# Kernel tuning notes

Measured on AMD Instinct MI355X. Metric: run time of the kernel, lower is better.

Reference implementation:

```python
import jax, jax.numpy as jnp
import numpy as np

N = 1024
FD = 40   # feat dim = out_dim1 + out_dim1//4
EPS = 1e-7


def _lin(key, din, dout):
    return jax.random.normal(key, (din, dout), jnp.float32) * (1.0 / np.sqrt(din))


def setup_inputs() -> dict:
    key = jax.random.key(0)
    ks = jax.random.split(key, 16)
    pc = jax.random.normal(ks[0], (1, N, 3), jnp.float32)
    nrm = jax.random.normal(ks[1], (1, N, 3), jnp.float32)
    pc_normal = nrm / (jnp.linalg.norm(nrm, axis=-1, keepdims=True) + EPS)
    feat = jax.random.normal(ks[2], (1, N, FD), jnp.float32) * 0.1
    # pairwise distance matrix, as precomputed upstream in the repo
    dist = jnp.linalg.norm(pc[:, :, None, :] - pc[:, None, :, :], axis=-1)
    z = lambda d: jnp.zeros((d,), jnp.float32)
    return {
        'pc': pc, 'pc_normal': pc_normal, 'dist': dist, 'feat': feat,
        'l0_fc0_w': _lin(ks[3], 84, 32), 'l0_fc0_b': z(32),
        'l0_fc1_w': _lin(ks[4], 84, 32), 'l0_fc1_b': z(32),
        'l0_fc2_w': _lin(ks[5], 32, 32), 'l0_fc2_b': z(32),
        'l1_fc1_w': _lin(ks[6], 32, 32), 'l1_fc1_b': z(32),
        'l1_fc2_w': _lin(ks[7], 32, 32), 'l1_fc2_b': z(32),
        'l2_fc0_w': _lin(ks[8], 32, 16), 'l2_fc0_b': z(16),
        'l2_fc1_w': _lin(ks[9], 32, 16), 'l2_fc1_b': z(16),
        'l2_fc2_w': _lin(ks[10], 16, 16), 'l2_fc2_b': z(16),
        'final_w': _lin(ks[11], 16, 66), 'final_b': z(66),
    }


def _res_layer(x, fc1w, fc1b, fc2w, fc2b, fc0w=None, fc0b=None):
    x_res = x if fc0w is None else x @ fc0w + fc0b
    h = jax.nn.relu(x @ fc1w + fc1b)
    return h @ fc2w + fc2b + x_res


def reference(pc, pc_normal, dist, feat,
              l0_fc0_w, l0_fc0_b, l0_fc1_w, l0_fc1_b, l0_fc2_w, l0_fc2_b,
              l1_fc1_w, l1_fc1_b, l1_fc2_w, l1_fc2_b,
              l2_fc0_w, l2_fc0_b, l2_fc1_w, l2_fc1_b, l2_fc2_w, l2_fc2_b,
              final_w, final_b):
    B, n, _ = pc.shape
    # pairwise displacement, normalized by precomputed dist (torch chunking is
    # pure memory management; the math over the full [B,N,N] block is identical)
    xx = pc[:, :, None, :] - pc[:, None, :, :]            # [B,N,N,3]
    xx_normed = xx / (dist[..., None] + EPS)
    n_i = pc_normal[:, :, None, :]                        # query normals
    n_j = pc_normal[:, None, :, :]                        # key normals
    ppf = jnp.concatenate([
        jnp.sum(n_i * xx_normed, -1, keepdims=True),
        jnp.sum(n_j * xx_normed, -1, keepdims=True),
        jnp.sum(n_i * n_j, -1, keepdims=True),
        dist[..., None],
    ], -1)                                                # [B,N,N,4]
    f_i = jnp.broadcast_to(feat[:, :, None, :], (B, n, n, FD))
    f_j = jnp.broadcast_to(feat[:, None, :, :], (B, n, n, FD))
    x = jnp.concatenate([f_i, f_j, ppf], -1)              # [B,N,N,84]
    x = _res_layer(x, l0_fc1_w, l0_fc1_b, l0_fc2_w, l0_fc2_b, l0_fc0_w, l0_fc0_b)
    x = _res_layer(x, l1_fc1_w, l1_fc1_b, l1_fc2_w, l1_fc2_b)
    x = _res_layer(x, l2_fc1_w, l2_fc1_b, l2_fc2_w, l2_fc2_b, l2_fc0_w, l2_fc0_b)
    return x @ final_w + final_b                          # [B,N,N,66]
```

## Files before the change

kernel.cpp:

```cpp
#include <hip/hip_runtime.h>
#include <hip/hip_bf16.h>

#define NPTS 1024
#define EPSF 1e-7f

typedef const float* fp;
typedef __attribute__((ext_vector_type(8))) short short8;
typedef __attribute__((ext_vector_type(4))) float float4v;

#define OFF_B0   32768
#define OFF_A1   65536
#define OFF_B1   98304
#define OFF_FRAG 131072
#define OFF_W0PT 134656
#define OFF_W1PT 134784

static __device__ __forceinline__ short f2bf(float x) {
    __hip_bfloat16 h = __float2bfloat16(x);
    short s; __builtin_memcpy(&s, &h, 2); return s;
}
static __device__ __forceinline__ void lds_fence() {
    __asm__ volatile("s_waitcnt lgkmcnt(0)" ::: "memory");
}

__global__ __launch_bounds__(128) void ppf_pre(
    fp feat, fp w0, fp b0, fp w1, fp b1,
    fp l0w2, fp l1w1, fp l1w2, fp l2w0, fp l2w1, fp l2w2, fp fw,
    float* __restrict__ ws)
{
    const int bid = blockIdx.x;
    const int t = threadIdx.x;
    if (bid < 1024) {
        __shared__ float f[40];
        int p = bid;
        if (t < 40) f[t] = feat[p * 40 + t];
        __syncthreads();
        int g = t >> 5;
        int c = t & 31;
        fp W = (g < 2) ? w0 : w1;
        int rowoff = (g & 1) ? 40 : 0;
        float acc = 0.f;
        if (!(g & 1)) acc = (g < 2) ? b0[c] : b1[c];
        #pragma unroll
        for (int k = 0; k < 40; ++k)
            acc += f[k] * W[(rowoff + k) * 32 + c];
        ws[g * 32768 + p * 32 + c] = acc;
    } else if (bid < 1038) {
        int ff = bid - 1024;
        if (t >= 64) return;
        const float* src; int Kr, Nw, n0;
        switch (ff) {
            case 0:  src = l0w2; Kr = 32; Nw = 32; n0 = 0;  break;
            case 1:  src = l0w2; Kr = 32; Nw = 32; n0 = 16; break;
            case 2:  src = l1w1; Kr = 32; Nw = 32; n0 = 0;  break;
            case 3:  src = l1w1; Kr = 32; Nw = 32; n0 = 16; break;
            case 4:  src = l1w2; Kr = 32; Nw = 32; n0 = 0;  break;
            case 5:  src = l1w2; Kr = 32; Nw = 32; n0 = 16; break;
            case 6:  src = l2w0; Kr = 32; Nw = 16; n0 = 0;  break;
            case 7:  src = l2w1; Kr = 32; Nw = 16; n0 = 0;  break;
            case 8:  src = l2w2; Kr = 16; Nw = 16; n0 = 0;  break;
            default: src = fw;   Kr = 16; Nw = 66; n0 = (ff - 9) * 16; break;
        }
        int q = t >> 4;
        int n = n0 + (t & 15);
        unsigned dw[4];
        #pragma unroll
        for (int w = 0; w < 4; ++w) {
            unsigned short e[2];
            #pragma unroll
            for (int v = 0; v < 2; ++v) {
                int k = q * 8 + w * 2 + v;
                float val = (k < Kr && n < Nw) ? src[k * Nw + n] : 0.f;
                short s = f2bf(val);
                __builtin_memcpy(&e[v], &s, 2);
            }
            dw[w] = (unsigned)e[0] | ((unsigned)e[1] << 16);
        }
        unsigned* dst = (unsigned*)ws + OFF_FRAG + ff * 256 + t * 4;
        #pragma unroll
        for (int w = 0; w < 4; ++w) dst[w] = dw[w];
    } else if (bid == 1038) {
        ws[OFF_W0PT + t] = w0[(80 + (t & 3)) * 32 + (t >> 2)];
    } else {
        ws[OFF_W1PT + t] = w1[(80 + (t & 3)) * 32 + (t >> 2)];
    }
}

static __device__ __forceinline__ float4v mfma16(short8 a, short8 b, float4v c) {
    return __builtin_amdgcn_mfma_f32_16x16x32_bf16(a, b, c, 0, 0, 0);
}

__global__ __launch_bounds__(256) void ppf_main(
    fp pc, fp nrm, fp dist,
    fp l0b2, fp l1b1, fp l1b2, fp l2b0, fp l2b1, fp l2b2, fp fb,
    const float* __restrict__ ws, float* __restrict__ out)
{
    __shared__ __align__(16) float lds[4 * 1152];
    const int tid  = threadIdx.x;
    const int wv   = tid >> 6;
    const int lane = tid & 63;
    const int q    = lane >> 4;
    const int ml   = lane & 15;
    const int kb   = q * 8;
    float* xt = &lds[wv * 1152];
    float* ht = xt + 576;

    const int i    = blockIdx.x >> 2;
    const int jblk = ((blockIdx.x & 3) << 8) + (wv << 6);

    const short8* fragp = (const short8*)(ws + OFF_FRAG);
    const short8 fg_l0w2_0 = fragp[0 * 64 + lane], fg_l0w2_1 = fragp[1 * 64 + lane];
    const short8 fg_l1w1_0 = fragp[2 * 64 + lane], fg_l1w1_1 = fragp[3 * 64 + lane];
    const short8 fg_l1w2_0 = fragp[4 * 64 + lane], fg_l1w2_1 = fragp[5 * 64 + lane];
    const short8 fg_l2w0   = fragp[6 * 64 + lane];
    const short8 fg_l2w1   = fragp[7 * 64 + lane];
    const short8 fg_l2w2   = fragp[8 * 64 + lane];
    const short8 fg_fw0 = fragp[9 * 64 + lane],  fg_fw1 = fragp[10 * 64 + lane];
    const short8 fg_fw2 = fragp[11 * 64 + lane], fg_fw3 = fragp[12 * 64 + lane];
    const short8 fg_fw4 = fragp[13 * 64 + lane];

    const float4v* a0p = (const float4v*)(ws + i * 32 + kb);
    const float4v a0lo = a0p[0], a0hi = a0p[1];
    const float4v* a1p = (const float4v*)(ws + OFF_A1 + i * 32 + kb);
    const float4v a1lo = a1p[0], a1hi = a1p[1];
    const float4v* b2p = (const float4v*)(l0b2 + kb);
    const float4v b2lo = b2p[0], b2hi = b2p[1];
    float4v w0t[8], w1t[8];
    {
        const float4v* w0ptp = (const float4v*)(ws + OFF_W0PT + kb * 4);
        const float4v* w1ptp = (const float4v*)(ws + OFF_W1PT + kb * 4);
        #pragma unroll
        for (int jj = 0; jj < 8; ++jj) { w0t[jj] = w0ptp[jj]; w1t[jj] = w1ptp[jj]; }
    }
    const float bl1b1_0 = l1b1[ml], bl1b1_1 = l1b1[16 + ml];
    const float bl1b2_0 = l1b2[ml], bl1b2_1 = l1b2[16 + ml];
    const float bl2b0 = l2b0[ml], bl2b1 = l2b1[ml], bl2b2 = l2b2[ml];
    float bfb[5];
    #pragma unroll
    for (int nt = 0; nt < 5; ++nt) { int c = nt * 16 + ml; bfb[nt] = (c < 66) ? fb[c] : 0.f; }

    const float pix = pc[i * 3], piy = pc[i * 3 + 1], piz = pc[i * 3 + 2];
    const float nix = nrm[i * 3], niy = nrm[i * 3 + 1], niz = nrm[i * 3 + 2];
    const float4v z4 = {0.f, 0.f, 0.f, 0.f};

    for (int tt = 0; tt < 4; ++tt) {
        const int j0 = jblk + tt * 16;
        const int jm = j0 + ml;

        const float d   = dist[i * NPTS + jm];
        const float inv = 1.f / (d + EPSF);
        const float dx = (pix - pc[jm * 3]) * inv;
        const float dy = (piy - pc[jm * 3 + 1]) * inv;
        const float dz = (piz - pc[jm * 3 + 2]) * inv;
        const float njx = nrm[jm * 3], njy = nrm[jm * 3 + 1], njz = nrm[jm * 3 + 2];
        const float p0 = nix * dx + niy * dy + niz * dz;
        const float p1 = njx * dx + njy * dy + njz * dz;
        const float p2 = nix * njx + niy * njy + niz * njz;
        const float p3 = d;

        const float4v* b0p = (const float4v*)(ws + OFF_B0 + jm * 32 + kb);
        const float4v b0lo = b0p[0], b0hi = b0p[1];
        const float4v* b1p = (const float4v*)(ws + OFF_B1 + jm * 32 + kb);
        const float4v b1lo = b1p[0], b1hi = b1p[1];

        float u0[8], u1[8];
        #pragma unroll
        for (int jj = 0; jj < 8; ++jj) {
            const float4v wa = w0t[jj], wb = w1t[jj];
            const float a0v = (jj < 4) ? a0lo[jj] : a0hi[jj - 4];
            const float a1v = (jj < 4) ? a1lo[jj] : a1hi[jj - 4];
            const float b0v = (jj < 4) ? b0lo[jj] : b0hi[jj - 4];
            const float b1v = (jj < 4) ? b1lo[jj] : b1hi[jj - 4];
            u0[jj] = a0v + b0v + p0 * wa.x + p1 * wa.y + p2 * wa.z + p3 * wa.w;
            u1[jj] = a1v + b1v + p0 * wb.x + p1 * wb.y + p2 * wb.z + p3 * wb.w;
        }

        short8 ha;
        #pragma unroll
        for (int jj = 0; jj < 8; ++jj) ha[jj] = f2bf(fmaxf(u1[jj], 0.f));
        float4v d0 = mfma16(ha, fg_l0w2_0, z4);
        float4v d1 = mfma16(ha, fg_l0w2_1, z4);

        #pragma unroll
        for (int rr = 0; rr < 4; ++rr) {
            xt[(q * 4 + rr) * 36 + ml]      = d0[rr];
            xt[(q * 4 + rr) * 36 + 16 + ml] = d1[rr];
        }
        lds_fence();
        float4v xalo = *(const float4v*)&xt[ml * 36 + kb];
        float4v xahi = *(const float4v*)&xt[ml * 36 + kb + 4];
        float x1a[8];
        #pragma unroll
        for (int jj = 0; jj < 8; ++jj) {
            const float dv = (jj < 4) ? xalo[jj] : xahi[jj - 4];
            const float bv = (jj < 4) ? b2lo[jj] : b2hi[jj - 4];
            x1a[jj] = dv + u0[jj] + bv;
        }
        float4v x1w0 = {x1a[0], x1a[1], x1a[2], x1a[3]};
        float4v x1w1 = {x1a[4], x1a[5], x1a[6], x1a[7]};
        *(float4v*)&xt[ml * 36 + kb]     = x1w0;
        *(float4v*)&xt[ml * 36 + kb + 4] = x1w1;
        lds_fence();

        short8 x1b;
        #pragma unroll
        for (int jj = 0; jj < 8; ++jj) x1b[jj] = f2bf(x1a[jj]);
        float4v ch0 = {bl1b1_0, bl1b1_0, bl1b1_0, bl1b1_0};
        float4v ch1 = {bl1b1_1, bl1b1_1, bl1b1_1, bl1b1_1};
        float4v dh0 = mfma16(x1b, fg_l1w1_0, ch0);
        float4v dh1 = mfma16(x1b, fg_l1w1_1, ch1);
        #pragma unroll
        for (int rr = 0; rr < 4; ++rr) {
            dh0[rr] = fmaxf(dh0[rr], 0.f);
            dh1[rr] = fmaxf(dh1[rr], 0.f);
            ht[(q * 4 + rr) * 36 + ml]      = dh0[rr];
            ht[(q * 4 + rr) * 36 + 16 + ml] = dh1[rr];
        }
        lds_fence();
        float4v hlo = *(const float4v*)&ht[ml * 36 + kb];
        float4v hhi = *(const float4v*)&ht[ml * 36 + kb + 4];
        short8 h1b;
        #pragma unroll
        for (int jj = 0; jj < 8; ++jj) h1b[jj] = f2bf((jj < 4) ? hlo[jj] : hhi[jj - 4]);
        float4v c20, c21;
        #pragma unroll
        for (int rr = 0; rr < 4; ++rr) {
            c20[rr] = xt[(q * 4 + rr) * 36 + ml]      + bl1b2_0;
            c21[rr] = xt[(q * 4 + rr) * 36 + 16 + ml] + bl1b2_1;
        }
        float4v dx20 = mfma16(h1b, fg_l1w2_0, c20);
        float4v dx21 = mfma16(h1b, fg_l1w2_1, c21);

        #pragma unroll
        for (int rr = 0; rr < 4; ++rr) {
            xt[(q * 4 + rr) * 36 + ml]      = dx20[rr];
            xt[(q * 4 + rr) * 36 + 16 + ml] = dx21[rr];
        }
        lds_fence();
        float4v x2lo = *(const float4v*)&xt[ml * 36 + kb];
        float4v x2hi = *(const float4v*)&xt[ml * 36 + kb + 4];
        short8 x2b;
        #pragma unroll
        for (int jj = 0; jj < 8; ++jj) x2b[jj] = f2bf((jj < 4) ? x2lo[jj] : x2hi[jj - 4]);

        float4v cr  = {bl2b0, bl2b0, bl2b0, bl2b0};
        float4v dr  = mfma16(x2b, fg_l2w0, cr);
        float4v cb  = {bl2b1, bl2b1, bl2b1, bl2b1};
        float4v dh2 = mfma16(x2b, fg_l2w1, cb);
        #pragma unroll
        for (int rr = 0; rr < 4; ++rr) {
            dh2[rr] = fmaxf(dh2[rr], 0.f);
            ht[(q * 4 + rr) * 36 + ml] = dh2[rr];
        }
        lds_fence();
        float4v h2lo = (q < 2) ? *(const float4v*)&ht[ml * 36 + kb]     : z4;
        float4v h2hi = (q < 2) ? *(const float4v*)&ht[ml * 36 + kb + 4] : z4;
        short8 h2b;
        #pragma unroll
        for (int jj = 0; jj < 8; ++jj) h2b[jj] = f2bf((jj < 4) ? h2lo[jj] : h2hi[jj - 4]);
        float4v c3;
        #pragma unroll
        for (int rr = 0; rr < 4; ++rr) c3[rr] = dr[rr] + bl2b2;
        float4v dx3 = mfma16(h2b, fg_l2w2, c3);

        #pragma unroll
        for (int rr = 0; rr < 4; ++rr) xt[(q * 4 + rr) * 36 + ml] = dx3[rr];
        lds_fence();
        float4v x3lo = (q < 2) ? *(const float4v*)&xt[ml * 36 + kb]     : z4;
        float4v x3hi = (q < 2) ? *(const float4v*)&xt[ml * 36 + kb + 4] : z4;
        short8 x3b;
        #pragma unroll
        for (int jj = 0; jj < 8; ++jj) x3b[jj] = f2bf((jj < 4) ? x3lo[jj] : x3hi[jj - 4]);
        float4v cf0 = {bfb[0], bfb[0], bfb[0], bfb[0]};
        float4v cf1 = {bfb[1], bfb[1], bfb[1], bfb[1]};
        float4v cf2 = {bfb[2], bfb[2], bfb[2], bfb[2]};
        float4v cf3 = {bfb[3], bfb[3], bfb[3], bfb[3]};
        float4v cf4 = {bfb[4], bfb[4], bfb[4], bfb[4]};
        float4v o0 = mfma16(x3b, fg_fw0, cf0);
        float4v o1 = mfma16(x3b, fg_fw1, cf1);
        float4v o2 = mfma16(x3b, fg_fw2, cf2);
        float4v o3 = mfma16(x3b, fg_fw3, cf3);
        float4v o4 = mfma16(x3b, fg_fw4, cf4);

        #pragma unroll
        for (int rr = 0; rr < 4; ++rr) {
            float* orow = out + (size_t)(i * NPTS + j0 + q * 4 + rr) * 66;
            orow[ml]      = o0[rr];
            orow[16 + ml] = o1[rr];
            orow[32 + ml] = o2[rr];
            orow[48 + ml] = o3[rr];
            if (ml < 2) orow[64 + ml] = o4[rr];
        }
    }
}

extern "C" void kernel_launch(void* const* d_in, const int* in_sizes, int n_in,
                              void* d_out, int out_size, void* d_ws, size_t ws_size,
                              hipStream_t stream) {
    (void)in_sizes; (void)n_in; (void)out_size; (void)ws_size;
    fp pc   = (fp)d_in[0];
    fp nrm  = (fp)d_in[1];
    fp dist = (fp)d_in[2];
    fp feat = (fp)d_in[3];
    fp w0   = (fp)d_in[4];   fp b0   = (fp)d_in[5];
    fp w1   = (fp)d_in[6];   fp b1   = (fp)d_in[7];
    fp l0w2 = (fp)d_in[8];   fp l0b2 = (fp)d_in[9];
    fp l1w1 = (fp)d_in[10];  fp l1b1 = (fp)d_in[11];
    fp l1w2 = (fp)d_in[12];  fp l1b2 = (fp)d_in[13];
    fp l2w0 = (fp)d_in[14];  fp l2b0 = (fp)d_in[15];
    fp l2w1 = (fp)d_in[16];  fp l2b1 = (fp)d_in[17];
    fp l2w2 = (fp)d_in[18];  fp l2b2 = (fp)d_in[19];
    fp fw   = (fp)d_in[20];  fp fb   = (fp)d_in[21];
    float* ws  = (float*)d_ws;
    float* out = (float*)d_out;

    ppf_pre<<<1040, 128, 0, stream>>>(feat, w0, b0, w1, b1,
        l0w2, l1w1, l1w2, l2w0, l2w1, l2w2, fw, ws);

    ppf_main<<<4096, 256, 0, stream>>>(pc, nrm, dist,
        l0b2, l1b1, l1b2, l2b0, l2b1, l2b2, fb, ws, out);
}
```

Baseline: 436.7 us.

## Transpose MFMA operands and permute weight fragments to drop LDS round-trips

Swaps the A/B operands of the hidden-layer MFMAs so that the transposed outputs land directly in the register layout the next MFMA needs as input. The weight fragments are prepacked with permuted columns to make this work. The per-layer shared-memory stores, fences and reloads are replaced by in-register bf16 packing, with a few cross-lane shuffles for the 16-wide layers. This removes LDS traffic and waitcnt stalls from the dependent chain, at the cost of more intricate index permutations that must stay exactly consistent.

```diff
diff --git a/kernel.cpp b/kernel.cpp
--- a/kernel.cpp
+++ b/kernel.cpp
@@ -19,9 +19,14 @@
     __hip_bfloat16 h = __float2bfloat16(x);
     short s; __builtin_memcpy(&s, &h, 2); return s;
 }
-static __device__ __forceinline__ void lds_fence() {
-    __asm__ volatile("s_waitcnt lgkmcnt(0)" ::: "memory");
-}
+static __device__ __forceinline__ unsigned pk2(float a, float b) {
+    short sa = f2bf(a), sb = f2bf(b);
+    unsigned short la, lb;
+    __builtin_memcpy(&la, &sa, 2); __builtin_memcpy(&lb, &sb, 2);
+    return (unsigned)la | ((unsigned)lb << 16);
+}
+
+union S8 { short8 s; unsigned u[4]; };
 
 __global__ __launch_bounds__(128) void ppf_pre(
     fp feat, fp w0, fp b0, fp w1, fp b1,
@@ -48,29 +53,34 @@
     } else if (bid < 1038) {
         int ff = bid - 1024;
         if (t >= 64) return;
-        const float* src; int Kr, Nw, n0;
+        const int p  = t & 15;
+        const int kq = t >> 4;
+        const float* src; int Kin, Nsrc, pm;
         switch (ff) {
-            case 0:  src = l0w2; Kr = 32; Nw = 32; n0 = 0;  break;
-            case 1:  src = l0w2; Kr = 32; Nw = 32; n0 = 16; break;
-            case 2:  src = l1w1; Kr = 32; Nw = 32; n0 = 0;  break;
-            case 3:  src = l1w1; Kr = 32; Nw = 32; n0 = 16; break;
-            case 4:  src = l1w2; Kr = 32; Nw = 32; n0 = 0;  break;
-            case 5:  src = l1w2; Kr = 32; Nw = 32; n0 = 16; break;
-            case 6:  src = l2w0; Kr = 32; Nw = 16; n0 = 0;  break;
-            case 7:  src = l2w1; Kr = 32; Nw = 16; n0 = 0;  break;
-            case 8:  src = l2w2; Kr = 16; Nw = 16; n0 = 0;  break;
-            default: src = fw;   Kr = 16; Nw = 66; n0 = (ff - 9) * 16; break;
-        }
-        int q = t >> 4;
-        int n = n0 + (t & 15);
+            case 0:  src = l0w2; Kin = 32; Nsrc = 32; pm = 1; break;
+            case 1:  src = l0w2; Kin = 32; Nsrc = 32; pm = 2; break;
+            case 2:  src = l1w1; Kin = 32; Nsrc = 32; pm = 1; break;
+            case 3:  src = l1w1; Kin = 32; Nsrc = 32; pm = 2; break;
+            case 4:  src = l1w2; Kin = 32; Nsrc = 32; pm = 1; break;
+            case 5:  src = l1w2; Kin = 32; Nsrc = 32; pm = 2; break;
+            case 6:  src = l2w0; Kin = 32; Nsrc = 16; pm = 3; break;
+            case 7:  src = l2w1; Kin = 32; Nsrc = 16; pm = 3; break;
+            case 8:  src = l2w2; Kin = 16; Nsrc = 16; pm = 3; break;
+            default: src = fw;   Kin = 16; Nsrc = 66; pm = 0; break;
+        }
+        int n;
+        if      (pm == 0) n = (ff - 9) * 16 + p;
+        else if (pm == 1) n = ((p >> 2) << 3) + (p & 3);
+        else if (pm == 2) n = ((p >> 2) << 3) + 4 + (p & 3);
+        else              n = (((p >> 2) & 1) << 3) + (((p >> 3) & 1) << 2) + (p & 3);
         unsigned dw[4];
         #pragma unroll
         for (int w = 0; w < 4; ++w) {
             unsigned short e[2];
             #pragma unroll
             for (int v = 0; v < 2; ++v) {
-                int k = q * 8 + w * 2 + v;
-                float val = (k < Kr && n < Nw) ? src[k * Nw + n] : 0.f;
+                int k = kq * 8 + w * 2 + v;
+                float val = (k < Kin && n < Nsrc) ? src[k * Nsrc + n] : 0.f;
                 short s = f2bf(val);
                 __builtin_memcpy(&e[v], &s, 2);
             }
@@ -95,26 +105,23 @@
     fp l0b2, fp l1b1, fp l1b2, fp l2b0, fp l2b1, fp l2b2, fp fb,
     const float* __restrict__ ws, float* __restrict__ out)
 {
-    __shared__ __align__(16) float lds[4 * 1152];
     const int tid  = threadIdx.x;
     const int wv   = tid >> 6;
     const int lane = tid & 63;
     const int q    = lane >> 4;
     const int ml   = lane & 15;
     const int kb   = q * 8;
-    float* xt = &lds[wv * 1152];
-    float* ht = xt + 576;
 
     const int i    = blockIdx.x >> 2;
     const int jblk = ((blockIdx.x & 3) << 8) + (wv << 6);
 
     const short8* fragp = (const short8*)(ws + OFF_FRAG);
-    const short8 fg_l0w2_0 = fragp[0 * 64 + lane], fg_l0w2_1 = fragp[1 * 64 + lane];
-    const short8 fg_l1w1_0 = fragp[2 * 64 + lane], fg_l1w1_1 = fragp[3 * 64 + lane];
-    const short8 fg_l1w2_0 = fragp[4 * 64 + lane], fg_l1w2_1 = fragp[5 * 64 + lane];
-    const short8 fg_l2w0   = fragp[6 * 64 + lane];
-    const short8 fg_l2w1   = fragp[7 * 64 + lane];
-    const short8 fg_l2w2   = fragp[8 * 64 + lane];
+    const short8 fa_l0w2_0 = fragp[0 * 64 + lane], fa_l0w2_1 = fragp[1 * 64 + lane];
+    const short8 fa_l1w1_0 = fragp[2 * 64 + lane], fa_l1w1_1 = fragp[3 * 64 + lane];
+    const short8 fa_l1w2_0 = fragp[4 * 64 + lane], fa_l1w2_1 = fragp[5 * 64 + lane];
+    const short8 fa_l2w0   = fragp[6 * 64 + lane];
+    const short8 fa_l2w1   = fragp[7 * 64 + lane];
+    const short8 fa_l2w2   = fragp[8 * 64 + lane];
     const short8 fg_fw0 = fragp[9 * 64 + lane],  fg_fw1 = fragp[10 * 64 + lane];
     const short8 fg_fw2 = fragp[11 * 64 + lane], fg_fw3 = fragp[12 * 64 + lane];
     const short8 fg_fw4 = fragp[13 * 64 + lane];
@@ -132,9 +139,14 @@
         #pragma unroll
         for (int jj = 0; jj < 8; ++jj) { w0t[jj] = w0ptp[jj]; w1t[jj] = w1ptp[jj]; }
     }
-    const float bl1b1_0 = l1b1[ml], bl1b1_1 = l1b1[16 + ml];
-    const float bl1b2_0 = l1b2[ml], bl1b2_1 = l1b2[16 + ml];
-    const float bl2b0 = l2b0[ml], bl2b1 = l2b1[ml], bl2b2 = l2b2[ml];
+    const float4v bA1lo = *(const float4v*)(l1b1 + kb);
+    const float4v bA1hi = *(const float4v*)(l1b1 + kb + 4);
+    const float4v bA2lo = *(const float4v*)(l1b2 + kb);
+    const float4v bA2hi = *(const float4v*)(l1b2 + kb + 4);
+    const int off16 = ((q & 1) << 3) + ((q >> 1) << 2);
+    const float4v b20v = *(const float4v*)(l2b0 + off16);
+    const float4v b21v = *(const float4v*)(l2b1 + off16);
+    const float4v b22v = *(const float4v*)(l2b2 + off16);
     float bfb[5];
     #pragma unroll
     for (int nt = 0; nt < 5; ++nt) { int c = nt * 16 + ml; bfb[nt] = (c < 66) ? fb[c] : 0.f; }
@@ -178,109 +190,70 @@
         short8 ha;
         #pragma unroll
         for (int jj = 0; jj < 8; ++jj) ha[jj] = f2bf(fmaxf(u1[jj], 0.f));
-        float4v d0 = mfma16(ha, fg_l0w2_0, z4);
-        float4v d1 = mfma16(ha, fg_l0w2_1, z4);
-
-        #pragma unroll
-        for (int rr = 0; rr < 4; ++rr) {
-            xt[(q * 4 + rr) * 36 + ml]      = d0[rr];
-            xt[(q * 4 + rr) * 36 + 16 + ml] = d1[rr];
-        }
-        lds_fence();
-        float4v xalo = *(const float4v*)&xt[ml * 36 + kb];
-        float4v xahi = *(const float4v*)&xt[ml * 36 + kb + 4];
+        float4v d0 = mfma16(fa_l0w2_0, ha, z4);
+        float4v d1 = mfma16(fa_l0w2_1, ha, z4);
+
         float x1a[8];
         #pragma unroll
-        for (int jj = 0; jj < 8; ++jj) {
-            const float dv = (jj < 4) ? xalo[jj] : xahi[jj - 4];
-            const float bv = (jj < 4) ? b2lo[jj] : b2hi[jj - 4];
-            x1a[jj] = dv + u0[jj] + bv;
-        }
-        float4v x1w0 = {x1a[0], x1a[1], x1a[2], x1a[3]};
-        float4v x1w1 = {x1a[4], x1a[5], x1a[6], x1a[7]};
-        *(float4v*)&xt[ml * 36 + kb]     = x1w0;
-        *(float4v*)&xt[ml * 36 + kb + 4] = x1w1;
-        lds_fence();
-
+        for (int jj = 0; jj < 4; ++jj) {
+            x1a[jj]     = d0[jj] + u0[jj]     + b2lo[jj];
+            x1a[4 + jj] = d1[jj] + u0[4 + jj] + b2hi[jj];
+        }
         short8 x1b;
         #pragma unroll
         for (int jj = 0; jj < 8; ++jj) x1b[jj] = f2bf(x1a[jj]);
-        float4v ch0 = {bl1b1_0, bl1b1_0, bl1b1_0, bl1b1_0};
-        float4v ch1 = {bl1b1_1, bl1b1_1, bl1b1_1, bl1b1_1};
-        float4v dh0 = mfma16(x1b, fg_l1w1_0, ch0);
-        float4v dh1 = mfma16(x1b, fg_l1w1_1, ch1);
-        #pragma unroll
-        for (int rr = 0; rr < 4; ++rr) {
-            dh0[rr] = fmaxf(dh0[rr], 0.f);
-            dh1[rr] = fmaxf(dh1[rr], 0.f);
-            ht[(q * 4 + rr) * 36 + ml]      = dh0[rr];
-            ht[(q * 4 + rr) * 36 + 16 + ml] = dh1[rr];
-        }
-        lds_fence();
-        float4v hlo = *(const float4v*)&ht[ml * 36 + kb];
-        float4v hhi = *(const float4v*)&ht[ml * 36 + kb + 4];
-        short8 h1b;
-        #pragma unroll
-        for (int jj = 0; jj < 8; ++jj) h1b[jj] = f2bf((jj < 4) ? hlo[jj] : hhi[jj - 4]);
+
+        float4v dh0 = mfma16(fa_l1w1_0, x1b, bA1lo);
+        float4v dh1 = mfma16(fa_l1w1_1, x1b, bA1hi);
+        short8 hb;
+        #pragma unroll
+        for (int rr = 0; rr < 4; ++rr) {
+            hb[rr]     = f2bf(fmaxf(dh0[rr], 0.f));
+            hb[4 + rr] = f2bf(fmaxf(dh1[rr], 0.f));
+        }
         float4v c20, c21;
         #pragma unroll
         for (int rr = 0; rr < 4; ++rr) {
-            c20[rr] = xt[(q * 4 + rr) * 36 + ml]      + bl1b2_0;
-            c21[rr] = xt[(q * 4 + rr) * 36 + 16 + ml] + bl1b2_1;
-        }
-        float4v dx20 = mfma16(h1b, fg_l1w2_0, c20);
-        float4v dx21 = mfma16(h1b, fg_l1w2_1, c21);
-
-        #pragma unroll
-        for (int rr = 0; rr < 4; ++rr) {
-            xt[(q * 4 + rr) * 36 + ml]      = dx20[rr];
-            xt[(q * 4 + rr) * 36 + 16 + ml] = dx21[rr];
-        }
-        lds_fence();
-        float4v x2lo = *(const float4v*)&xt[ml * 36 + kb];
-        float4v x2hi = *(const float4v*)&xt[ml * 36 + kb + 4];
+            c20[rr] = x1a[rr]     + bA2lo[rr];
+            c21[rr] = x1a[4 + rr] + bA2hi[rr];
+        }
+        float4v dx20 = mfma16(fa_l1w2_0, hb, c20);
+        float4v dx21 = mfma16(fa_l1w2_1, hb, c21);
         short8 x2b;
         #pragma unroll
-        for (int jj = 0; jj < 8; ++jj) x2b[jj] = f2bf((jj < 4) ? x2lo[jj] : x2hi[jj - 4]);
-
-        float4v cr  = {bl2b0, bl2b0, bl2b0, bl2b0};
-        float4v dr  = mfma16(x2b, fg_l2w0, cr);
-        float4v cb  = {bl2b1, bl2b1, bl2b1, bl2b1};
-        float4v dh2 = mfma16(x2b, fg_l2w1, cb);
-        #pragma unroll
-        for (int rr = 0; rr < 4; ++rr) {
-            dh2[rr] = fmaxf(dh2[rr], 0.f);
-            ht[(q * 4 + rr) * 36 + ml] = dh2[rr];
-        }
-        lds_fence();
-        float4v h2lo = (q < 2) ? *(const float4v*)&ht[ml * 36 + kb]     : z4;
-        float4v h2hi = (q < 2) ? *(const float4v*)&ht[ml * 36 + kb + 4] : z4;
-        short8 h2b;
-        #pragma unroll
-        for (int jj = 0; jj < 8; ++jj) h2b[jj] = f2bf((jj < 4) ? h2lo[jj] : h2hi[jj - 4]);
+        for (int rr = 0; rr < 4; ++rr) {
+            x2b[rr]     = f2bf(dx20[rr]);
+            x2b[4 + rr] = f2bf(dx21[rr]);
+        }
+
+        float4v dr  = mfma16(fa_l2w0, x2b, b20v);
+        float4v dh2 = mfma16(fa_l2w1, x2b, b21v);
+        unsigned p01 = pk2(fmaxf(dh2[0], 0.f), fmaxf(dh2[1], 0.f));
+        unsigned p23 = pk2(fmaxf(dh2[2], 0.f), fmaxf(dh2[3], 0.f));
+        unsigned q01 = __shfl_xor(p01, 32);
+        unsigned q23 = __shfl_xor(p23, 32);
+        S8 h2u; h2u.u[0] = p01; h2u.u[1] = p23; h2u.u[2] = q01; h2u.u[3] = q23;
         float4v c3;
         #pragma unroll
-        for (int rr = 0; rr < 4; ++rr) c3[rr] = dr[rr] + bl2b2;
-        float4v dx3 = mfma16(h2b, fg_l2w2, c3);
-
-        #pragma unroll
-        for (int rr = 0; rr < 4; ++rr) xt[(q * 4 + rr) * 36 + ml] = dx3[rr];
-        lds_fence();
-        float4v x3lo = (q < 2) ? *(const float4v*)&xt[ml * 36 + kb]     : z4;
-        float4v x3hi = (q < 2) ? *(const float4v*)&xt[ml * 36 + kb + 4] : z4;
-        short8 x3b;
-        #pragma unroll
-        for (int jj = 0; jj < 8; ++jj) x3b[jj] = f2bf((jj < 4) ? x3lo[jj] : x3hi[jj - 4]);
+        for (int rr = 0; rr < 4; ++rr) c3[rr] = dr[rr] + b22v[rr];
+        float4v dx3 = mfma16(fa_l2w2, h2u.s, c3);
+
+        unsigned r01 = pk2(dx3[0], dx3[1]);
+        unsigned r23 = pk2(dx3[2], dx3[3]);
+        unsigned s01 = __shfl_xor(r01, 32);
+        unsigned s23 = __shfl_xor(r23, 32);
+        S8 x3u; x3u.u[0] = r01; x3u.u[1] = r23; x3u.u[2] = s01; x3u.u[3] = s23;
+
         float4v cf0 = {bfb[0], bfb[0], bfb[0], bfb[0]};
         float4v cf1 = {bfb[1], bfb[1], bfb[1], bfb[1]};
         float4v cf2 = {bfb[2], bfb[2], bfb[2], bfb[2]};
         float4v cf3 = {bfb[3], bfb[3], bfb[3], bfb[3]};
         float4v cf4 = {bfb[4], bfb[4], bfb[4], bfb[4]};
-        float4v o0 = mfma16(x3b, fg_fw0, cf0);
-        float4v o1 = mfma16(x3b, fg_fw1, cf1);
-        float4v o2 = mfma16(x3b, fg_fw2, cf2);
-        float4v o3 = mfma16(x3b, fg_fw3, cf3);
-        float4v o4 = mfma16(x3b, fg_fw4, cf4);
+        float4v o0 = mfma16(x3u.s, fg_fw0, cf0);
+        float4v o1 = mfma16(x3u.s, fg_fw1, cf1);
+        float4v o2 = mfma16(x3u.s, fg_fw2, cf2);
+        float4v o3 = mfma16(x3u.s, fg_fw3, cf3);
+        float4v o4 = mfma16(x3u.s, fg_fw4, cf4);
 
         #pragma unroll
         for (int rr = 0; rr < 4; ++rr) {
```

Result: faster. 388.0 us (-11.1%).
